# Performance work log

Hardware: AMD Instinct MI355X
Metric: run time of the kernel (lower is better)

## Reference

```python
import jax, jax.numpy as jnp
import numpy as np

N, F, H = 4096, 512, 64
TEMP = 1.0
EPS = 1e-6


def _lin_init(k, fi, fo):
    s = 1.0 / np.sqrt(fi)
    return jax.random.uniform(k, (fi, fo), jnp.float32, -s, s)


def setup_inputs() -> dict:
    key = jax.random.key(0)
    ks = jax.random.split(key, 8)
    adj = jax.random.uniform(ks[0], (N, N), jnp.float32)
    adj = 0.5 * (adj + adj.T)  # symmetric dense adjacency
    x = jax.random.normal(ks[1], (N, F), jnp.float32)
    return {
        'adj': adj,
        'x': x,
        'Wg': _lin_init(ks[2], F, H), 'bg': jnp.zeros((H,), jnp.float32),
        'Wa1': _lin_init(ks[3], H, H), 'ba1': jnp.zeros((H,), jnp.float32),
        'Wa2': _lin_init(ks[4], H, F), 'ba2': jnp.zeros((F,), jnp.float32),
        'Wx1': _lin_init(ks[5], H, H), 'bx1': jnp.zeros((H,), jnp.float32),
        'Wx2': _lin_init(ks[6], H, F), 'bx2': jnp.zeros((F,), jnp.float32),
    }


def _relaxed_bernoulli_st(probs, noise_logistic, temp):
    # pyro RelaxedBernoulliStraightThrough.rsample(): gumbel-sigmoid + hard round w/ ST grad
    p = jnp.clip(probs, EPS, 1.0 - EPS)
    logits = jnp.log(p) - jnp.log1p(-p)
    soft = jax.nn.sigmoid((logits + noise_logistic) / temp)
    hard = jnp.round(soft)
    return soft + jax.lax.stop_gradient(hard - soft)


def _logistic_noise(k, shape):
    u = jax.random.uniform(k, shape, jnp.float32, EPS, 1.0 - EPS)
    return jnp.log(u) - jnp.log1p(-u)


def reference(adj, x, Wg, bg, Wa1, ba1, Wa2, ba2, Wx1, bx1, Wx2, bx2):
    nkey = jax.random.key(42)
    k1, k2 = jax.random.split(nkey)
    # GCN_Body, 1 layer (dropout is eval no-op): h = relu(A @ (X W) + b)
    h = jax.nn.relu(adj @ (x @ Wg) + bg)            # [N, H]
    # MLPA: Z = Linear(ReLU(Linear(h)))
    Z = jax.nn.relu(h @ Wa1 + ba1) @ Wa2 + ba2      # [N, F]
    adj_logits = Z @ Z.T                            # [N, N]
    edge_probs = jax.nn.sigmoid(adj_logits)
    a = _relaxed_bernoulli_st(edge_probs, _logistic_noise(k1, (N, N)), TEMP)
    a = jnp.triu(a, 1)
    a = a + a.T
    # normalize_adj: fill_diagonal_(1); D^{-1/2} A D^{-1/2} (diag matmuls == row/col scaling)
    i = jnp.arange(N)
    a = a.at[i, i].set(1.0)
    d = a.sum(1) ** -0.5                            # [N]
    adj_norm = d[:, None] * a * d[None, :]
    # MLPX feature mask
    mask_logits = jax.nn.relu(h @ Wx1 + bx1) @ Wx2 + bx2  # [N, F]
    mask_probs = jax.nn.sigmoid(mask_logits)
    mask = _relaxed_bernoulli_st(mask_probs, _logistic_noise(k2, (N, F)), TEMP)
    x_new = x * mask
    return (adj_norm, x_new, adj_logits)
```

## Files before the change

kernel.cpp:

```cpp
#include <hip/hip_runtime.h>
#include <cstdint>
#include <cmath>

#define NN 4096
#define FF 512
#define HH 64
#define KSPLIT 8

typedef unsigned short ushort_t;
typedef short bf16x8 __attribute__((ext_vector_type(8)));
typedef float f32x4 __attribute__((ext_vector_type(4)));

__host__ __device__ __forceinline__ uint32_t rotl32(uint32_t x, int r) {
    return (x << r) | (x >> (32 - r));
}

__host__ __device__ __forceinline__ void threefry2x32(uint32_t ks0, uint32_t ks1,
                                                      uint32_t x0, uint32_t x1,
                                                      uint32_t& o0, uint32_t& o1) {
    uint32_t ks2 = ks0 ^ ks1 ^ 0x1BD11BDAu;
    x0 += ks0; x1 += ks1;
    x0 += x1; x1 = rotl32(x1, 13); x1 ^= x0;
    x0 += x1; x1 = rotl32(x1, 15); x1 ^= x0;
    x0 += x1; x1 = rotl32(x1, 26); x1 ^= x0;
    x0 += x1; x1 = rotl32(x1,  6); x1 ^= x0;
    x0 += ks1; x1 += ks2 + 1u;
    x0 += x1; x1 = rotl32(x1, 17); x1 ^= x0;
    x0 += x1; x1 = rotl32(x1, 29); x1 ^= x0;
    x0 += x1; x1 = rotl32(x1, 16); x1 ^= x0;
    x0 += x1; x1 = rotl32(x1, 24); x1 ^= x0;
    x0 += ks2; x1 += ks0 + 2u;
    x0 += x1; x1 = rotl32(x1, 13); x1 ^= x0;
    x0 += x1; x1 = rotl32(x1, 15); x1 ^= x0;
    x0 += x1; x1 = rotl32(x1, 26); x1 ^= x0;
    x0 += x1; x1 = rotl32(x1,  6); x1 ^= x0;
    x0 += ks0; x1 += ks1 + 3u;
    x0 += x1; x1 = rotl32(x1, 17); x1 ^= x0;
    x0 += x1; x1 = rotl32(x1, 29); x1 ^= x0;
    x0 += x1; x1 = rotl32(x1, 16); x1 ^= x0;
    x0 += x1; x1 = rotl32(x1, 24); x1 ^= x0;
    x0 += ks1; x1 += ks2 + 4u;
    x0 += x1; x1 = rotl32(x1, 13); x1 ^= x0;
    x0 += x1; x1 = rotl32(x1, 15); x1 ^= x0;
    x0 += x1; x1 = rotl32(x1, 26); x1 ^= x0;
    x0 += x1; x1 = rotl32(x1,  6); x1 ^= x0;
    x0 += ks2; x1 += ks0 + 5u;
    o0 = x0; o1 = x1;
}

__device__ __forceinline__ uint32_t jax_bits32(uint32_t k0, uint32_t k1, uint32_t j) {
    uint32_t b0, b1;
    threefry2x32(k0, k1, 0u, j, b0, b1);
    return b0 ^ b1;
}

__device__ __forceinline__ float jax_uniform(uint32_t bits) {
    const float minv = 1e-6f;
    const float maxv = (float)(1.0 - 1e-6);
    const float span = maxv - minv;
    float f = __uint_as_float((bits >> 9) | 0x3f800000u) - 1.0f;
    float u = __fadd_rn(__fmul_rn(f, span), minv);
    return fmaxf(minv, u);
}

__device__ __forceinline__ float hard_sample_f(float l, float u) {
    float thr = 1.0f / (1.0f + expf(l));
    return (u > thr) ? 1.0f : 0.0f;
}

__device__ __forceinline__ ushort_t f32_to_bf16_rne(float f) {
    uint32_t x = __float_as_uint(f);
    uint32_t r = (x + 0x7fffu + ((x >> 16) & 1u)) >> 16;
    return (ushort_t)r;
}


__global__ void k_xw(const float* __restrict__ x, const float* __restrict__ Wg,
                     float* __restrict__ T) {
    int col = threadIdx.x;
    int row = blockIdx.x * 4 + threadIdx.y;
    const float* xr = x + row * FF;
    float acc = 0.0f;
    #pragma unroll 4
    for (int k = 0; k < FF; ++k)
        acc += xr[k] * Wg[k * HH + col];
    T[row * HH + col] = acc;
}

__global__ void __launch_bounds__(256)
k_adjT2(const float* __restrict__ adj, const float* __restrict__ T,
        float* __restrict__ partial) {
    __shared__ __align__(16) float As[64][68];
    __shared__ __align__(16) float Ts[64][64];
    int t = threadIdx.x;
    int tx = t & 15, ty = t >> 4;
    int r0 = blockIdx.x * 64;
    int kb = blockIdx.y * (NN / KSPLIT);
    float acc[4][4] = {};
    for (int k0 = 0; k0 < NN / KSPLIT; k0 += 64) {
        __syncthreads();
        for (int n = t; n < 1024; n += 256) {
            int rr = n >> 4, kq = n & 15;
            float4 v = *(const float4*)&adj[(size_t)(r0 + rr) * NN + kb + k0 + kq * 4];
            *(float4*)&As[rr][kq * 4] = v;
        }
        for (int n = t; n < 1024; n += 256) {
            int rr = n >> 4, kq = n & 15;
            float4 v = *(const float4*)&T[(size_t)(kb + k0 + rr) * HH + kq * 4];
            *(float4*)&Ts[rr][kq * 4] = v;
        }
        __syncthreads();
        for (int kk = 0; kk < 64; ++kk) {
            float a[4];
            #pragma unroll
            for (int i = 0; i < 4; ++i) a[i] = As[ty * 4 + i][kk];
            float4 bv = *(float4*)&Ts[kk][tx * 4];
            float b[4] = {bv.x, bv.y, bv.z, bv.w};
            #pragma unroll
            for (int i = 0; i < 4; ++i)
                #pragma unroll
                for (int j = 0; j < 4; ++j)
                    acc[i][j] += a[i] * b[j];
        }
    }
    float* P = partial + (size_t)blockIdx.y * NN * HH;
    #pragma unroll
    for (int i = 0; i < 4; ++i) {
        int row = r0 + ty * 4 + i;
        float4 v = {acc[i][0], acc[i][1], acc[i][2], acc[i][3]};
        *(float4*)&P[(size_t)row * HH + tx * 4] = v;
    }
}

__global__ void k_hred(const float* __restrict__ partial, const float* __restrict__ bg,
                       float* __restrict__ h) {
    int idx = blockIdx.x * 256 + threadIdx.x;
    float s = 0.0f;
    #pragma unroll
    for (int p = 0; p < KSPLIT; ++p) s += partial[(size_t)p * NN * HH + idx];
    float v = s + bg[idx & (HH - 1)];
    h[idx] = v > 0.0f ? v : 0.0f;
}

__global__ void k_small64(const float* __restrict__ A, const float* __restrict__ W,
                          const float* __restrict__ b, float* __restrict__ O) {
    __shared__ float Wl[HH][HH];
    int tx = threadIdx.x, ty = threadIdx.y;
    int tid = ty * 64 + tx;
    for (int n = tid; n < HH * HH; n += 256)
        ((float*)Wl)[n] = W[n];
    __syncthreads();
    int row = blockIdx.x * 4 + ty;
    const float* Ar = A + row * HH;
    float acc = 0.0f;
    #pragma unroll
    for (int k = 0; k < HH; ++k) acc += Ar[k] * Wl[k][tx];
    float v = acc + b[tx];
    O[row * HH + tx] = v > 0.0f ? v : 0.0f;
}

__global__ void k_projZ(const float* __restrict__ A, const float* __restrict__ W,
                        const float* __restrict__ b, ushort_t* __restrict__ Zb) {
    int tx = threadIdx.x, ty = threadIdx.y;
    int row = blockIdx.y * 4 + ty;
    int col = blockIdx.x * 64 + tx;
    const float* Ar = A + row * HH;
    float acc = 0.0f;
    #pragma unroll
    for (int k = 0; k < HH; ++k) acc += Ar[k] * W[k * FF + col];
    Zb[(size_t)row * FF + col] = f32_to_bf16_rne(acc + b[col]);
}

__global__ void k_mask(const float* __restrict__ M1, const float* __restrict__ W,
                       const float* __restrict__ b, const float* __restrict__ x,
                       float* __restrict__ xnew, uint32_t k20, uint32_t k21,
                       float Lmin, float Lmax) {
    int tx = threadIdx.x, ty = threadIdx.y;
    int row = blockIdx.y * 4 + ty;
    int col = blockIdx.x * 64 + tx;
    const float* Ar = M1 + row * HH;
    float acc = 0.0f;
    #pragma unroll
    for (int k = 0; k < HH; ++k) acc += Ar[k] * W[k * FF + col];
    float ml = acc + b[col];
    float l = ml < Lmin ? Lmin : (ml > Lmax ? Lmax : ml);
    uint32_t idx = (uint32_t)row * FF + (uint32_t)col;
    float u = jax_uniform(jax_bits32(k20, k21, idx));
    float m = hard_sample_f(l, u);
    xnew[idx] = (m != 0.0f) ? x[idx] : 0.0f;
}

__global__ void __launch_bounds__(256)
k_zzt_gemm(const ushort_t* __restrict__ Zb, float* __restrict__ out2) {
    __shared__ __align__(16) ushort_t At[128][72];
    __shared__ __align__(16) ushort_t Bt[128][72];
    int t = threadIdx.x;
    int lane = t & 63, w = t >> 6;
    int lr = lane & 15, lk = lane >> 4;
    int b = blockIdx.x;
    int bi = b >> 5, bj = b & 31;
    int rbase = bi * 128, cbase = bj * 128;
    f32x4 acc[2][8] = {};
    for (int k0 = 0; k0 < FF; k0 += 64) {
        __syncthreads();
        for (int n = t; n < 1024; n += 256) {
            int rr = n >> 3, ck = n & 7;
            *(uint4*)&At[rr][ck * 8] = *(const uint4*)&Zb[(size_t)(rbase + rr) * FF + k0 + ck * 8];
            *(uint4*)&Bt[rr][ck * 8] = *(const uint4*)&Zb[(size_t)(cbase + rr) * FF + k0 + ck * 8];
        }
        __syncthreads();
        #pragma unroll
        for (int ks = 0; ks < 2; ++ks) {
            bf16x8 a0 = *(const bf16x8*)&At[w * 32 + lr][ks * 32 + lk * 8];
            bf16x8 a1 = *(const bf16x8*)&At[w * 32 + 16 + lr][ks * 32 + lk * 8];
            #pragma unroll
            for (int j = 0; j < 8; ++j) {
                bf16x8 bb = *(const bf16x8*)&Bt[j * 16 + lr][ks * 32 + lk * 8];
                acc[0][j] = __builtin_amdgcn_mfma_f32_16x16x32_bf16(a0, bb, acc[0][j], 0, 0, 0);
                acc[1][j] = __builtin_amdgcn_mfma_f32_16x16x32_bf16(a1, bb, acc[1][j], 0, 0, 0);
            }
        }
    }
    #pragma unroll
    for (int it = 0; it < 2; ++it) {
        int rg = rbase + w * 32 + it * 16 + lk * 4;
        #pragma unroll
        for (int reg = 0; reg < 4; ++reg) {
            #pragma unroll
            for (int j = 0; j < 8; ++j) {
                out2[(size_t)(rg + reg) * NN + cbase + j * 16 + lr] = acc[it][j][reg];
            }
        }
    }
}

__global__ void __launch_bounds__(256)
k_sample(const float* __restrict__ out2, uint32_t* __restrict__ mask,
         float* __restrict__ rowsum, uint32_t k10, uint32_t k11,
         float Lmin, float Lmax) {
    int g = blockIdx.x * 256 + threadIdx.x;
    int r = g >> 7;
    int wd = g & 127;
    const float* zr = out2 + (size_t)r * NN + wd * 32;
    uint32_t word = 0;
    #pragma unroll
    for (int q = 0; q < 8; ++q) {
        float4 zv = *(const float4*)&zr[q * 4];
        float za[4] = {zv.x, zv.y, zv.z, zv.w};
        #pragma unroll
        for (int e4 = 0; e4 < 4; ++e4) {
            int e = q * 4 + e4;
            int c = wd * 32 + e;
            float z = za[e4];
            float l = z < Lmin ? Lmin : (z > Lmax ? Lmax : z);
            int lo = r < c ? r : c;
            int hi = r < c ? c : r;
            uint32_t idx = (uint32_t)lo * NN + (uint32_t)hi;
            float u = jax_uniform(jax_bits32(k10, k11, idx));
            float thr = 1.0f / (1.0f + expf(l));
            uint32_t bit = (r == c) ? 1u : (u > thr ? 1u : 0u);
            word |= bit << e;
        }
    }
    mask[g] = word;
    int pc = __popc(word);
    #pragma unroll
    for (int off = 32; off; off >>= 1) pc += __shfl_down(pc, off);
    if ((threadIdx.x & 63) == 0) atomicAdd(&rowsum[r], (float)pc);
}

__global__ void k_deg(const float* __restrict__ rowsum, float* __restrict__ dvec) {
    int i = blockIdx.x * 256 + threadIdx.x;
    dvec[i] = 1.0f / sqrtf(rowsum[i]);
}

__global__ void k_scale2(const uint32_t* __restrict__ mask,
                         const float* __restrict__ dvec, float* __restrict__ out0) {
    size_t idx = ((size_t)blockIdx.x * 256 + threadIdx.x) * 4;
    int r = (int)(idx >> 12);
    int c = (int)(idx & 4095);
    uint32_t wv = mask[idx >> 5];
    int sh = (int)(idx & 31);
    float dr = dvec[r];
    float4 dc = *(const float4*)&dvec[c];
    float4 o;
    o.x = ((wv >> (sh + 0)) & 1u) ? dr * dc.x : 0.0f;
    o.y = ((wv >> (sh + 1)) & 1u) ? dr * dc.y : 0.0f;
    o.z = ((wv >> (sh + 2)) & 1u) ? dr * dc.z : 0.0f;
    o.w = ((wv >> (sh + 3)) & 1u) ? dr * dc.w : 0.0f;
    *(float4*)&out0[idx] = o;
}

extern "C" void kernel_launch(void* const* d_in, const int* in_sizes, int n_in,
                              void* d_out, int out_size, void* d_ws, size_t ws_size,
                              hipStream_t stream) {
    const float* adj = (const float*)d_in[0];
    const float* x   = (const float*)d_in[1];
    const float* Wg  = (const float*)d_in[2];
    const float* bg  = (const float*)d_in[3];
    const float* Wa1 = (const float*)d_in[4];
    const float* ba1 = (const float*)d_in[5];
    const float* Wa2 = (const float*)d_in[6];
    const float* ba2 = (const float*)d_in[7];
    const float* Wx1 = (const float*)d_in[8];
    const float* bx1 = (const float*)d_in[9];
    const float* Wx2 = (const float*)d_in[10];
    const float* bx2 = (const float*)d_in[11];

    float* out0 = (float*)d_out;
    float* out1 = out0 + (size_t)NN * NN;
    float* out2 = out1 + (size_t)NN * FF;

    float* T       = (float*)d_ws;
    float* h       = T + NN * HH;
    float* A1      = h + NN * HH;
    float* M1      = A1 + NN * HH;
    ushort_t* Zb   = (ushort_t*)(M1 + NN * HH);
    float* partial = (float*)(Zb + (size_t)NN * FF);
    float* dvec    = partial + (size_t)KSPLIT * NN * HH;
    float* rowsum  = dvec + NN;
    uint32_t* mask = (uint32_t*)partial;

    uint32_t k1a, k1b, k2a, k2b;
    threefry2x32(0u, 42u, 0u, 0u, k1a, k1b);
    threefry2x32(0u, 42u, 0u, 1u, k2a, k2b);

    const float Lmax = (float)(std::log(1.0 - 1e-6) - std::log1p(-(1.0 - 1e-6)));
    const float Lmin = (float)(std::log(1e-6) - std::log1p(-1e-6));

    k_xw<<<NN / 4, dim3(64, 4), 0, stream>>>(x, Wg, T);
    k_adjT2<<<dim3(64, KSPLIT), 256, 0, stream>>>(adj, T, partial);
    k_hred<<<NN * HH / 256, 256, 0, stream>>>(partial, bg, h);
    k_small64<<<NN / 4, dim3(64, 4), 0, stream>>>(h, Wa1, ba1, A1);
    k_projZ<<<dim3(FF / 64, NN / 4), dim3(64, 4), 0, stream>>>(A1, Wa2, ba2, Zb);

    k_zzt_gemm<<<1024, 256, 0, stream>>>(Zb, out2);

    hipMemsetAsync(rowsum, 0, NN * sizeof(float), stream);
    k_sample<<<NN * NN / 32 / 256, 256, 0, stream>>>(out2, mask, rowsum,
                                                     k1a, k1b, Lmin, Lmax);
    k_deg<<<NN / 256, 256, 0, stream>>>(rowsum, dvec);
    k_scale2<<<NN * NN / 4 / 256, 256, 0, stream>>>(mask, dvec, out0);

    k_small64<<<NN / 4, dim3(64, 4), 0, stream>>>(h, Wx1, bx1, M1);
    k_mask<<<dim3(FF / 64, NN / 4), dim3(64, 4), 0, stream>>>(M1, Wx2, bx2, x, out1,
                                                              k2a, k2b, Lmin, Lmax);
}
```

Before: 462.6 us.

## Exploit symmetry: compute upper-triangular tiles of ZZ^T and sampling, mirror results

The Z·Zᵀ GEMM now launches only the 528 upper-triangular 128×128 tiles and writes each off-diagonal tile twice, once directly and once transposed through shared memory. The sampling kernel likewise handles only upper-triangular tiles. It computes the threefry random bits once per symmetric pair, transposes the mask bit-words through LDS, and accumulates row and column degree sums with shared atomics before the global atomics. This roughly halves the MFMA work and the RNG/exp work. In exchange it adds a transposed store pass and lower parallelism (528 blocks instead of 1024 and 2048).

After: 443.0 us. 1.04x faster.

```diff
diff --git a/kernel.cpp b/kernel.cpp
--- a/kernel.cpp
+++ b/kernel.cpp
@@ -191,31 +191,34 @@
 }
 
 __global__ void __launch_bounds__(256)
-k_zzt_gemm(const ushort_t* __restrict__ Zb, float* __restrict__ out2) {
-    __shared__ __align__(16) ushort_t At[128][72];
-    __shared__ __align__(16) ushort_t Bt[128][72];
+k_zzt_gemm_tri(const ushort_t* __restrict__ Zb, float* __restrict__ out2) {
+    __shared__ __align__(16) union {
+        struct { ushort_t At[128][72]; ushort_t Bt[128][72]; } s;
+        float Tls[32][132];
+    } sm;
     int t = threadIdx.x;
     int lane = t & 63, w = t >> 6;
     int lr = lane & 15, lk = lane >> 4;
-    int b = blockIdx.x;
-    int bi = b >> 5, bj = b & 31;
+    int b = blockIdx.x, bi = 0;
+    while (b >= 32 - bi) { b -= 32 - bi; ++bi; }
+    int bj = bi + b;
     int rbase = bi * 128, cbase = bj * 128;
     f32x4 acc[2][8] = {};
     for (int k0 = 0; k0 < FF; k0 += 64) {
         __syncthreads();
         for (int n = t; n < 1024; n += 256) {
             int rr = n >> 3, ck = n & 7;
-            *(uint4*)&At[rr][ck * 8] = *(const uint4*)&Zb[(size_t)(rbase + rr) * FF + k0 + ck * 8];
-            *(uint4*)&Bt[rr][ck * 8] = *(const uint4*)&Zb[(size_t)(cbase + rr) * FF + k0 + ck * 8];
+            *(uint4*)&sm.s.At[rr][ck * 8] = *(const uint4*)&Zb[(size_t)(rbase + rr) * FF + k0 + ck * 8];
+            *(uint4*)&sm.s.Bt[rr][ck * 8] = *(const uint4*)&Zb[(size_t)(cbase + rr) * FF + k0 + ck * 8];
         }
         __syncthreads();
         #pragma unroll
         for (int ks = 0; ks < 2; ++ks) {
-            bf16x8 a0 = *(const bf16x8*)&At[w * 32 + lr][ks * 32 + lk * 8];
-            bf16x8 a1 = *(const bf16x8*)&At[w * 32 + 16 + lr][ks * 32 + lk * 8];
+            bf16x8 a0 = *(const bf16x8*)&sm.s.At[w * 32 + lr][ks * 32 + lk * 8];
+            bf16x8 a1 = *(const bf16x8*)&sm.s.At[w * 32 + 16 + lr][ks * 32 + lk * 8];
             #pragma unroll
             for (int j = 0; j < 8; ++j) {
-                bf16x8 bb = *(const bf16x8*)&Bt[j * 16 + lr][ks * 32 + lk * 8];
+                bf16x8 bb = *(const bf16x8*)&sm.s.Bt[j * 16 + lr][ks * 32 + lk * 8];
                 acc[0][j] = __builtin_amdgcn_mfma_f32_16x16x32_bf16(a0, bb, acc[0][j], 0, 0, 0);
                 acc[1][j] = __builtin_amdgcn_mfma_f32_16x16x32_bf16(a1, bb, acc[1][j], 0, 0, 0);
             }
@@ -225,48 +228,101 @@
     for (int it = 0; it < 2; ++it) {
         int rg = rbase + w * 32 + it * 16 + lk * 4;
         #pragma unroll
-        for (int reg = 0; reg < 4; ++reg) {
-            #pragma unroll
-            for (int j = 0; j < 8; ++j) {
+        for (int reg = 0; reg < 4; ++reg)
+            #pragma unroll
+            for (int j = 0; j < 8; ++j)
                 out2[(size_t)(rg + reg) * NN + cbase + j * 16 + lr] = acc[it][j][reg];
+    }
+    if (bi != bj) {
+        #pragma unroll
+        for (int g = 0; g < 4; ++g) {
+            __syncthreads();
+            #pragma unroll
+            for (int it = 0; it < 2; ++it)
+                #pragma unroll
+                for (int jp = 0; jp < 2; ++jp)
+                    #pragma unroll
+                    for (int reg = 0; reg < 4; ++reg)
+                        sm.Tls[jp * 16 + lr][w * 32 + it * 16 + lk * 4 + reg] =
+                            acc[it][g * 2 + jp][reg];
+            __syncthreads();
+            #pragma unroll
+            for (int r4 = 0; r4 < 4; ++r4) {
+                int tr = r4 * 8 + (t >> 5);
+                int tc = (t & 31) * 4;
+                float4 v = *(const float4*)&sm.Tls[tr][tc];
+                *(float4*)&out2[(size_t)(cbase + g * 32 + tr) * NN + rbase + tc] = v;
             }
         }
     }
 }
 
 __global__ void __launch_bounds__(256)
-k_sample(const float* __restrict__ out2, uint32_t* __restrict__ mask,
-         float* __restrict__ rowsum, uint32_t k10, uint32_t k11,
-         float Lmin, float Lmax) {
-    int g = blockIdx.x * 256 + threadIdx.x;
-    int r = g >> 7;
-    int wd = g & 127;
-    const float* zr = out2 + (size_t)r * NN + wd * 32;
-    uint32_t word = 0;
-    #pragma unroll
-    for (int q = 0; q < 8; ++q) {
-        float4 zv = *(const float4*)&zr[q * 4];
-        float za[4] = {zv.x, zv.y, zv.z, zv.w};
+k_sample_tri(const float* __restrict__ out2, uint32_t* __restrict__ mask,
+             float* __restrict__ rowsum, uint32_t k10, uint32_t k11,
+             float Lmin, float Lmax) {
+    __shared__ uint32_t Wl[128][5];
+    __shared__ int rs[128], cs[128];
+    int t = threadIdx.x;
+    int b = blockIdx.x, bi = 0;
+    while (b >= 32 - bi) { b -= 32 - bi; ++bi; }
+    int bj = bi + b;
+    int rbase = bi * 128, cbase = bj * 128;
+    if (t < 128) { rs[t] = 0; cs[t] = 0; }
+    __syncthreads();
+    int rr = t >> 1;
+    int r = rbase + rr;
+    int rowacc = 0;
+    #pragma unroll
+    for (int wi = 0; wi < 2; ++wi) {
+        int wc = (t & 1) * 2 + wi;
+        const float* zr = out2 + (size_t)r * NN + cbase + wc * 32;
+        uint32_t word = 0;
         #pragma unroll
-        for (int e4 = 0; e4 < 4; ++e4) {
-            int e = q * 4 + e4;
-            int c = wd * 32 + e;
-            float z = za[e4];
-            float l = z < Lmin ? Lmin : (z > Lmax ? Lmax : z);
-            int lo = r < c ? r : c;
-            int hi = r < c ? c : r;
-            uint32_t idx = (uint32_t)lo * NN + (uint32_t)hi;
-            float u = jax_uniform(jax_bits32(k10, k11, idx));
-            float thr = 1.0f / (1.0f + expf(l));
-            uint32_t bit = (r == c) ? 1u : (u > thr ? 1u : 0u);
-            word |= bit << e;
-        }
-    }
-    mask[g] = word;
-    int pc = __popc(word);
-    #pragma unroll
-    for (int off = 32; off; off >>= 1) pc += __shfl_down(pc, off);
-    if ((threadIdx.x & 63) == 0) atomicAdd(&rowsum[r], (float)pc);
+        for (int q = 0; q < 8; ++q) {
+            float4 zv = *(const float4*)&zr[q * 4];
+            float za[4] = {zv.x, zv.y, zv.z, zv.w};
+            #pragma unroll
+            for (int e4 = 0; e4 < 4; ++e4) {
+                int e = q * 4 + e4;
+                int c = cbase + wc * 32 + e;
+                float z = za[e4];
+                float l = z < Lmin ? Lmin : (z > Lmax ? Lmax : z);
+                int lo = r < c ? r : c;
+                int hi = r < c ? c : r;
+                uint32_t idx = (uint32_t)lo * NN + (uint32_t)hi;
+                float u = jax_uniform(jax_bits32(k10, k11, idx));
+                float thr = 1.0f / (1.0f + expf(l));
+                uint32_t bit = (r == c) ? 1u : (u > thr ? 1u : 0u);
+                word |= bit << e;
+            }
+        }
+        Wl[rr][wc] = word;
+        mask[(size_t)r * (NN / 32) + ((cbase >> 5) + wc)] = word;
+        rowacc += __popc(word);
+    }
+    atomicAdd(&rs[rr], rowacc);
+    __syncthreads();
+    if (bi != bj) {
+        int cc = t >> 1;
+        int colacc = 0;
+        #pragma unroll
+        for (int wi = 0; wi < 2; ++wi) {
+            int wr = (t & 1) * 2 + wi;
+            uint32_t tw = 0;
+            #pragma unroll
+            for (int bb = 0; bb < 32; ++bb)
+                tw |= ((Wl[wr * 32 + bb][cc >> 5] >> (cc & 31)) & 1u) << bb;
+            mask[(size_t)(cbase + cc) * (NN / 32) + ((rbase >> 5) + wr)] = tw;
+            colacc += __popc(tw);
+        }
+        atomicAdd(&cs[cc], colacc);
+    }
+    __syncthreads();
+    if (t < 128) {
+        atomicAdd(&rowsum[rbase + t], (float)rs[t]);
+        if (bi != bj) atomicAdd(&rowsum[cbase + t], (float)cs[t]);
+    }
 }
 
 __global__ void k_deg(const float* __restrict__ rowsum, float* __restrict__ dvec) {
@@ -334,11 +390,10 @@
     k_small64<<<NN / 4, dim3(64, 4), 0, stream>>>(h, Wa1, ba1, A1);
     k_projZ<<<dim3(FF / 64, NN / 4), dim3(64, 4), 0, stream>>>(A1, Wa2, ba2, Zb);
 
-    k_zzt_gemm<<<1024, 256, 0, stream>>>(Zb, out2);
+    k_zzt_gemm_tri<<<528, 256, 0, stream>>>(Zb, out2);
 
     hipMemsetAsync(rowsum, 0, NN * sizeof(float), stream);
-    k_sample<<<NN * NN / 32 / 256, 256, 0, stream>>>(out2, mask, rowsum,
-                                                     k1a, k1b, Lmin, Lmax);
+    k_sample_tri<<<528, 256, 0, stream>>>(out2, mask, rowsum, k1a, k1b, Lmin, Lmax);
     k_deg<<<NN / 256, 256, 0, stream>>>(rowsum, dvec);
     k_scale2<<<NN * NN / 4 / 256, 256, 0, stream>>>(mask, dvec, out0);
 
```
